# Kernel tuning notes

Hardware: AMD Instinct MI355X
Metric: run time of the kernel (lower is better)

Reference implementation:

```python
import jax, jax.numpy as jnp
import numpy as np

SEQ, BATCH, INPUT = 2048, 64, 16
HEADS, HID = 8, 64  # per-head hidden = hidden_size/output_size = 512/8


def setup_inputs() -> dict:
    key = jax.random.key(0)
    ks = jax.random.split(key, 8)
    s = 1.0 / np.sqrt(HID)  # PyTorch LSTM/Linear init scale
    return {
        "x": jax.random.normal(ks[0], (SEQ, BATCH, INPUT), jnp.float32),
        "W_ih": jax.random.uniform(ks[1], (HEADS, 4 * HID, INPUT), jnp.float32, -s, s),
        "W_hh": jax.random.uniform(ks[2], (HEADS, 4 * HID, HID), jnp.float32, -s, s),
        "b_ih": jax.random.uniform(ks[3], (HEADS, 4 * HID), jnp.float32, -s, s),
        "b_hh": jax.random.uniform(ks[4], (HEADS, 4 * HID), jnp.float32, -s, s),
        "W_lin": jax.random.uniform(ks[5], (HEADS, HID), jnp.float32, -s, s),
        "b_lin": jax.random.uniform(ks[6], (HEADS,), jnp.float32, -s, s),
    }


def _multihead_lstm(x, W_ih, W_hh, b_ih, b_hh):
    # x: (T,B,I); weights stacked over heads H. PyTorch gate order: i,f,g,o.
    T, B = x.shape[0], x.shape[1]
    H, G = W_hh.shape[0], W_hh.shape[1]  # G = 4*hid
    hid = G // 4
    # Input projection for all timesteps/heads at once: (T,B,H,4h)
    xp = jnp.einsum("tbi,hgi->tbhg", x, W_ih) + b_ih + b_hh

    def step(carry, xt):
        h_prev, c_prev = carry  # (B,H,hid)
        z = xt + jnp.einsum("bhk,hgk->bhg", h_prev, W_hh)  # (B,H,4h)
        i = jax.nn.sigmoid(z[..., 0 * hid:1 * hid])
        f = jax.nn.sigmoid(z[..., 1 * hid:2 * hid])
        g = jnp.tanh(z[..., 2 * hid:3 * hid])
        o = jax.nn.sigmoid(z[..., 3 * hid:4 * hid])
        c = f * c_prev + i * g
        h = o * jnp.tanh(c)
        return (h, c), h

    zeros = jnp.zeros((B, H, hid), x.dtype)
    _, hs = jax.lax.scan(step, (zeros, zeros), xp)  # hs: (T,B,H,hid)
    return hs


def reference(x, W_ih, W_hh, b_ih, b_hh, W_lin, b_lin):
    hs = _multihead_lstm(x, W_ih, W_hh, b_ih, b_hh)  # (T,B,H,hid)
    # per-head Linear(hid -> 1), concatenated over heads -> (T,B,H)
    out = jnp.einsum("tbhk,hk->tbh", hs, W_lin) + b_lin
    # lstm_output accumulates (sums) the per-head hidden trajectories
    lstm_output = hs.sum(axis=2)  # (T,B,hid)
    return out, lstm_output
```

## Files before the change

### kernel.cpp

```cpp
#include <hip/hip_runtime.h>
#include <hip/hip_fp16.h>

#define TT   2048
#define BB   64
#define II   16
#define HH   8
#define HIDN 64
#define GG   256
#define T4   (TT / 4)

typedef _Float16 h2 __attribute__((ext_vector_type(2)));
typedef _Float16 h4 __attribute__((ext_vector_type(4)));
typedef _Float16 h8 __attribute__((ext_vector_type(8)));

__device__ __forceinline__ float fdot2(h2 a, h2 b, float c) {
    return __builtin_amdgcn_fdot2(a, b, c, false);
}
__device__ __forceinline__ float fast_sigmoid(float z) {
    return __builtin_amdgcn_rcpf(1.0f + __expf(-z));
}
__device__ __forceinline__ float fast_tanh(float z) {
    return fmaf(2.0f, __builtin_amdgcn_rcpf(1.0f + __expf(-2.0f * z)), -1.0f);
}

__global__ void cvt_x_kernel(const float* __restrict__ x, _Float16* __restrict__ xh, int n4) {
    int i = blockIdx.x * blockDim.x + threadIdx.x;
    if (i < n4) {
        float4 v = ((const float4*)x)[i];
        ((h2*)xh)[2 * i]     = h2{ (_Float16)v.x, (_Float16)v.y };
        ((h2*)xh)[2 * i + 1] = h2{ (_Float16)v.z, (_Float16)v.w };
    }
}

__global__ __launch_bounds__(64, 1)
void lstm_rl(const _Float16* __restrict__ xh,
             const float* __restrict__ Wih,
             const float* __restrict__ Whh,
             const float* __restrict__ bih,
             const float* __restrict__ bhh,
             _Float16* __restrict__ stage_f16)
{
    const int lane = threadIdx.x;
    const int c    = blockIdx.x;
    const int b    = c & (BB - 1);
    const int hd   = c >> 6;
    const bool odd = lane & 1;

    h2 whh[4][HIDN / 2];
    h2 wih[4][II / 2];
    float bias[4];
#pragma unroll
    for (int g = 0; g < 4; ++g) {
        const int r = hd * GG + g * HIDN + lane;
        const float4* p = (const float4*)(Whh + (size_t)r * HIDN);
#pragma unroll
        for (int q = 0; q < HIDN / 4; ++q) {
            float4 v = p[q];
            whh[g][2 * q]     = h2{ (_Float16)v.x, (_Float16)v.y };
            whh[g][2 * q + 1] = h2{ (_Float16)v.z, (_Float16)v.w };
        }
        const float4* pi = (const float4*)(Wih + (size_t)r * II);
#pragma unroll
        for (int q = 0; q < II / 4; ++q) {
            float4 v = pi[q];
            wih[g][2 * q]     = h2{ (_Float16)v.x, (_Float16)v.y };
            wih[g][2 * q + 1] = h2{ (_Float16)v.z, (_Float16)v.w };
        }
        bias[g] = bih[r] + bhh[r];
    }

    float cst   = 0.0f;
    int  packed = 0;

    const _Float16* xhp = xh + b * II;
    h2 xv[II / 2], xn[II / 2];
    auto ldx = [&](int t, h2* dst) {
        const h8* p = (const h8*)(xhp + (size_t)t * BB * II);
        union { h8 v; h2 p2[4]; } u0, u1;
        u0.v = p[0];
        u1.v = p[1];
#pragma unroll
        for (int i = 0; i < 4; ++i) { dst[i] = u0.p2[i]; dst[4 + i] = u1.p2[i]; }
    };
    ldx(0, xv);

    h4* sptr = (h4*)(stage_f16 + (size_t)c * 256 + lane * 4);

    for (int t4 = 0; t4 < T4; ++t4) {
        union { h4 v4; _Float16 e[4]; } hpk;
#pragma unroll
        for (int j = 0; j < 4; ++j) {
            const int t = t4 * 4 + j;
            ldx(t + 1, xn);

            float z0 = bias[0], z1 = bias[1], z2 = bias[2], z3 = bias[3];
#pragma unroll
            for (int q = 0; q < II / 2; ++q) {
                z0 = fdot2(wih[0][q], xv[q], z0);
                z1 = fdot2(wih[1][q], xv[q], z1);
                z2 = fdot2(wih[2][q], xv[q], z2);
                z3 = fdot2(wih[3][q], xv[q], z3);
            }
#pragma unroll
            for (int q = 0; q < HIDN / 2; ++q) {
                h2 hq = __builtin_bit_cast(h2,
                            __builtin_amdgcn_readlane(packed, 2 * q));
                z0 = fdot2(whh[0][q], hq, z0);
                z1 = fdot2(whh[1][q], hq, z1);
                z2 = fdot2(whh[2][q], hq, z2);
                z3 = fdot2(whh[3][q], hq, z3);
            }

            float gi = fast_sigmoid(z0);
            float gf = fast_sigmoid(z1);
            float gg = fast_tanh(z2);
            float go = fast_sigmoid(z3);

            cst = fmaf(gf, cst, gi * gg);
            float hv = go * fast_tanh(cst);
            _Float16 h16 = (_Float16)hv;
            hpk.e[j] = h16;

            int h32 = (int)__builtin_bit_cast(unsigned short, h16);
            int hsw = __builtin_amdgcn_mov_dpp(h32, 0xB1, 0xF, 0xF, true);
            int lo  = odd ? hsw : h32;
            int hi  = odd ? h32 : hsw;
            packed  = lo | (hi << 16);

#pragma unroll
            for (int q = 0; q < II / 2; ++q) xv[q] = xn[q];
        }
        *sptr = hpk.v4;
        sptr += 512 * 64;
    }
}

template <int STAGE, bool XF16>
__global__ __launch_bounds__(64, 1)
void lstm_wave(const float* __restrict__ x,
               const _Float16* __restrict__ xh,
               const float* __restrict__ Wih,
               const float* __restrict__ Whh,
               const float* __restrict__ bih,
               const float* __restrict__ bhh,
               const float* __restrict__ Wlin,
               const float* __restrict__ blin,
               float* __restrict__ out,
               float* __restrict__ lstm_out,
               _Float16* __restrict__ stage_f16)
{
    const int lane = threadIdx.x;
    const int c    = blockIdx.x;
    const int b    = c & (BB - 1);
    const int hd   = c >> 6;

    h2 whh[4][HIDN / 2];
    h2 wih[4][II / 2];
    float bias[4];
#pragma unroll
    for (int g = 0; g < 4; ++g) {
        const int r = hd * GG + g * HIDN + lane;
        const float4* p = (const float4*)(Whh + (size_t)r * HIDN);
#pragma unroll
        for (int q = 0; q < HIDN / 4; ++q) {
            float4 v = p[q];
            whh[g][2 * q]     = h2{ (_Float16)v.x, (_Float16)v.y };
            whh[g][2 * q + 1] = h2{ (_Float16)v.z, (_Float16)v.w };
        }
        const float4* pi = (const float4*)(Wih + (size_t)r * II);
#pragma unroll
        for (int q = 0; q < II / 4; ++q) {
            float4 v = pi[q];
            wih[g][2 * q]     = h2{ (_Float16)v.x, (_Float16)v.y };
            wih[g][2 * q + 1] = h2{ (_Float16)v.z, (_Float16)v.w };
        }
        bias[g] = bih[r] + bhh[r];
    }
    float wl = 0.0f, blv = 0.0f;
    if (STAGE == 2) { wl = Wlin[hd * HIDN + lane]; blv = blin[hd]; }

    __shared__ __align__(16) _Float16 hbuf[HIDN];
    hbuf[lane] = (_Float16)0.0f;

    float cst = 0.0f;

    const _Float16* xhp = xh + b * II;
    const float*    xfp = x + b * II;
    h2 xv[II / 2];
    auto load_x = [&](int t, h2* dst) {
        int tc = t < TT ? t : TT - 1;
        if (XF16) {
            const h8* p = (const h8*)(xhp + (size_t)tc * BB * II);
            union { h8 v; h2 p2[4]; } u0, u1;
            u0.v = p[0];
            u1.v = p[1];
#pragma unroll
            for (int i = 0; i < 4; ++i) { dst[i] = u0.p2[i]; dst[4 + i] = u1.p2[i]; }
        } else {
            const float4* p = (const float4*)(xfp + (size_t)tc * BB * II);
#pragma unroll
            for (int q = 0; q < 4; ++q) {
                float4 v = p[q];
                dst[2 * q]     = h2{ (_Float16)v.x, (_Float16)v.y };
                dst[2 * q + 1] = h2{ (_Float16)v.z, (_Float16)v.w };
            }
        }
    };
    load_x(0, xv);

    h4* sptr = (h4*)(stage_f16 + (size_t)c * 256 + lane * 4);

    for (int t4 = 0; t4 < T4; ++t4) {
        union { h4 v4; h2 p2[2]; } hp;
#pragma unroll
        for (int j = 0; j < 4; ++j) {
            const int t = t4 * 4 + j;
            h2 xn[II / 2];
            load_x(t + 1, xn);

            union { h8 v[8]; h2 p[32]; } hr;
#pragma unroll
            for (int q = 0; q < 8; ++q) hr.v[q] = ((const h8*)hbuf)[q];

            float z0 = bias[0], z1 = bias[1], z2 = bias[2], z3 = bias[3];
#pragma unroll
            for (int q = 0; q < HIDN / 2; ++q) {
                z0 = fdot2(whh[0][q], hr.p[q], z0);
                z1 = fdot2(whh[1][q], hr.p[q], z1);
                z2 = fdot2(whh[2][q], hr.p[q], z2);
                z3 = fdot2(whh[3][q], hr.p[q], z3);
            }
#pragma unroll
            for (int q = 0; q < II / 2; ++q) {
                z0 = fdot2(wih[0][q], xv[q], z0);
                z1 = fdot2(wih[1][q], xv[q], z1);
                z2 = fdot2(wih[2][q], xv[q], z2);
                z3 = fdot2(wih[3][q], xv[q], z3);
            }

            float gi = fast_sigmoid(z0);
            float gf = fast_sigmoid(z1);
            float gg = fast_tanh(z2);
            float go = fast_sigmoid(z3);

            cst = fmaf(gf, cst, gi * gg);
            float h = go * fast_tanh(cst);
            _Float16 h16 = (_Float16)h;

            hbuf[lane] = h16;
            hp.p2[j >> 1][j & 1] = h16;

            if (STAGE == 2) {
                atomicAdd(&lstm_out[((size_t)t * BB + b) * HIDN + lane], h);
                float p = h * wl;
                p += __shfl_down(p, 32, 64);
                p += __shfl_down(p, 16, 64);
                p += __shfl_down(p, 8, 64);
                p += __shfl_down(p, 4, 64);
                p += __shfl_down(p, 2, 64);
                p += __shfl_down(p, 1, 64);
                if (lane == 0) out[((size_t)t * BB + b) * HH + hd] = p + blv;
            }

#pragma unroll
            for (int q = 0; q < II / 2; ++q) xv[q] = xn[q];
        }
        if (STAGE == 1) {
            *sptr = hp.v4;
            sptr += 512 * 64;
        }
    }
}

__global__ __launch_bounds__(256)
void pass_lstm(const _Float16* __restrict__ stage, float* __restrict__ lstm_out)
{
    const int tid  = threadIdx.x;
    const int k    = tid & (HIDN - 1);
    const int q    = tid >> 6;
    const int b    = blockIdx.x & (BB - 1);
    const int tile = blockIdx.x >> 6;
    const h4* sp = (const h4*)stage;

#pragma unroll
    for (int g = 0; g < 4; ++g) {
        const int t4 = tile * 16 + q + 4 * g;
        float acc0 = 0.f, acc1 = 0.f, acc2 = 0.f, acc3 = 0.f;
#pragma unroll
        for (int hd = 0; hd < HH; ++hd) {
            h4 v = sp[((size_t)t4 * 512 + hd * 64 + b) * 64 + k];
            acc0 += (float)v.x; acc1 += (float)v.y;
            acc2 += (float)v.z; acc3 += (float)v.w;
        }
        const size_t t = (size_t)t4 * 4;
        lstm_out[((t + 0) * BB + b) * HIDN + k] = acc0;
        lstm_out[((t + 1) * BB + b) * HIDN + k] = acc1;
        lstm_out[((t + 2) * BB + b) * HIDN + k] = acc2;
        lstm_out[((t + 3) * BB + b) * HIDN + k] = acc3;
    }
}

__global__ __launch_bounds__(512)
void pass_out(const _Float16* __restrict__ stage,
              const float* __restrict__ Wlin,
              const float* __restrict__ blin,
              float* __restrict__ out)
{
    __shared__ float wls[GG * 2];
    const int tid = threadIdx.x;
    wls[tid] = Wlin[tid];
    __syncthreads();

    const int b  = tid >> 3;
    const int hd = tid & 7;
    const int c  = hd * 64 + b;
    const int t4 = blockIdx.x;
    const float bl = blin[hd];

    const h4* sp = (const h4*)stage + ((size_t)t4 * 512 + c) * 64;
    float a0 = 0.f, a1 = 0.f, a2 = 0.f, a3 = 0.f;
#pragma unroll 8
    for (int k = 0; k < HIDN; ++k) {
        h4 v = sp[k];
        float w = wls[hd * HIDN + k];
        a0 = fmaf((float)v.x, w, a0);
        a1 = fmaf((float)v.y, w, a1);
        a2 = fmaf((float)v.z, w, a2);
        a3 = fmaf((float)v.w, w, a3);
    }
    const size_t t = (size_t)t4 * 4;
    out[(t + 0) * 512 + tid] = a0 + bl;
    out[(t + 1) * 512 + tid] = a1 + bl;
    out[(t + 2) * 512 + tid] = a2 + bl;
    out[(t + 3) * 512 + tid] = a3 + bl;
}

extern "C" void kernel_launch(void* const* d_in, const int* in_sizes, int n_in,
                              void* d_out, int out_size, void* d_ws, size_t ws_size,
                              hipStream_t stream)
{
    const float* x    = (const float*)d_in[0];
    const float* Wih  = (const float*)d_in[1];
    const float* Whh  = (const float*)d_in[2];
    const float* bih  = (const float*)d_in[3];
    const float* bhh  = (const float*)d_in[4];
    const float* Wlin = (const float*)d_in[5];
    const float* blin = (const float*)d_in[6];

    float* out  = (float*)d_out;
    float* lstm = out + (size_t)TT * BB * HH;

    const size_t xbytes = (size_t)TT * BB * II * 2 + 4096;
    const size_t slab16 = (size_t)TT * BB * HH * HIDN * 2;

    const bool xf16 = ws_size >= xbytes;
    _Float16* xh = (_Float16*)d_ws;
    char* slabp  = (char*)d_ws + (xf16 ? xbytes : 0);
    size_t avail = ws_size - (xf16 ? xbytes : 0);
    const int mode = (avail >= slab16) ? 1 : 2;

    if (xf16) {
        int n4 = TT * BB * II / 4;
        cvt_x_kernel<<<(n4 + 255) / 256, 256, 0, stream>>>(x, xh, n4);
    }

    _Float16* sh = (_Float16*)slabp;

    if (mode == 1 && xf16) {
        lstm_rl<<<dim3(BB * HH), dim3(64), 0, stream>>>(xh, Wih, Whh, bih, bhh, sh);
        pass_lstm<<<dim3(BB * 32), dim3(256), 0, stream>>>(sh, lstm);
        pass_out <<<dim3(T4), dim3(512), 0, stream>>>(sh, Wlin, blin, out);
    } else if (mode == 1) {
        dim3 grid(BB * HH), block(64);
        lstm_wave<1, false><<<grid, block, 0, stream>>>(x, xh, Wih, Whh, bih, bhh,
                                                        Wlin, blin, out, lstm, sh);
        pass_lstm<<<dim3(BB * 32), dim3(256), 0, stream>>>(sh, lstm);
        pass_out <<<dim3(T4), dim3(512), 0, stream>>>(sh, Wlin, blin, out);
    } else {
        hipMemsetAsync(lstm, 0, (size_t)TT * BB * HIDN * 4, stream);
        dim3 grid(BB * HH), block(64);
        if (xf16)
            lstm_wave<2, true><<<grid, block, 0, stream>>>(x, xh, Wih, Whh, bih, bhh,
                                                           Wlin, blin, out, lstm, sh);
        else
            lstm_wave<2, false><<<grid, block, 0, stream>>>(x, xh, Wih, Whh, bih, bhh,
                                                            Wlin, blin, out, lstm, sh);
    }
}
```

Before: 1.169 ms.

## Broadcast hidden state through LDS and precompute next-step input projection

Replaces the per-step readlane broadcast of the packed hidden state with a write to a small shared-memory buffer that every lane reads back as vector loads. It also computes the next timestep's input projection right after the state update, taking it off the critical recurrence path. The dot-product chains are split into two accumulators to shorten dependency latency. The block pads its LDS to about 64 KB, apparently to limit how many blocks share a CU. The code has no barrier between the LDS write and the next read; it relies on the 64-thread block being a single wavefront executing in lockstep.

Measured after the change: 1.086 ms. 7.1% less time.

```diff
diff --git a/kernel.cpp b/kernel.cpp
--- a/kernel.cpp
+++ b/kernel.cpp
@@ -32,19 +32,25 @@
     }
 }
 
+struct SmemPad {
+    _Float16 hbuf[HIDN];
+    char     pad[63872];
+};
+
 __global__ __launch_bounds__(64, 1)
-void lstm_rl(const _Float16* __restrict__ xh,
-             const float* __restrict__ Wih,
-             const float* __restrict__ Whh,
-             const float* __restrict__ bih,
-             const float* __restrict__ bhh,
-             _Float16* __restrict__ stage_f16)
+void lstm_reg(const _Float16* __restrict__ xh,
+              const float* __restrict__ Wih,
+              const float* __restrict__ Whh,
+              const float* __restrict__ bih,
+              const float* __restrict__ bhh,
+              _Float16* __restrict__ stage_f16)
 {
     const int lane = threadIdx.x;
     const int c    = blockIdx.x;
     const int b    = c & (BB - 1);
     const int hd   = c >> 6;
-    const bool odd = lane & 1;
+
+    __shared__ __align__(16) SmemPad smem;
 
     h2 whh[4][HIDN / 2];
     h2 wih[4][II / 2];
@@ -69,11 +75,13 @@
         bias[g] = bih[r] + bhh[r];
     }
 
-    float cst   = 0.0f;
-    int  packed = 0;
+    smem.hbuf[lane] = (_Float16)0.0f;
+    if (lane == 0) smem.pad[0] = 1;
+
+    float cst = 0.0f;
 
     const _Float16* xhp = xh + b * II;
-    h2 xv[II / 2], xn[II / 2];
+    h2 xn[II / 2];
     auto ldx = [&](int t, h2* dst) {
         const h8* p = (const h8*)(xhp + (size_t)t * BB * II);
         union { h8 v; h2 p2[4]; } u0, u1;
@@ -82,7 +90,19 @@
 #pragma unroll
         for (int i = 0; i < 4; ++i) { dst[i] = u0.p2[i]; dst[4 + i] = u1.p2[i]; }
     };
-    ldx(0, xv);
+
+    float xzA[4], xzB[4];
+    ldx(0, xn);
+#pragma unroll
+    for (int g = 0; g < 4; ++g) { xzA[g] = bias[g]; xzB[g] = 0.0f; }
+#pragma unroll
+    for (int q = 0; q < 4; ++q)
+#pragma unroll
+        for (int g = 0; g < 4; ++g) xzA[g] = fdot2(wih[g][q], xn[q], xzA[g]);
+#pragma unroll
+    for (int q = 4; q < 8; ++q)
+#pragma unroll
+        for (int g = 0; g < 4; ++g) xzB[g] = fdot2(wih[g][q], xn[q], xzB[g]);
 
     h4* sptr = (h4*)(stage_f16 + (size_t)c * 256 + lane * 4);
 
@@ -91,25 +111,31 @@
 #pragma unroll
         for (int j = 0; j < 4; ++j) {
             const int t = t4 * 4 + j;
+
+            union { h8 v[8]; h2 p[32]; } hr;
+#pragma unroll
+            for (int q = 0; q < 8; ++q) hr.v[q] = ((const h8*)smem.hbuf)[q];
+
             ldx(t + 1, xn);
 
-            float z0 = bias[0], z1 = bias[1], z2 = bias[2], z3 = bias[3];
-#pragma unroll
-            for (int q = 0; q < II / 2; ++q) {
-                z0 = fdot2(wih[0][q], xv[q], z0);
-                z1 = fdot2(wih[1][q], xv[q], z1);
-                z2 = fdot2(wih[2][q], xv[q], z2);
-                z3 = fdot2(wih[3][q], xv[q], z3);
-            }
-#pragma unroll
-            for (int q = 0; q < HIDN / 2; ++q) {
-                h2 hq = __builtin_bit_cast(h2,
-                            __builtin_amdgcn_readlane(packed, 2 * q));
-                z0 = fdot2(whh[0][q], hq, z0);
-                z1 = fdot2(whh[1][q], hq, z1);
-                z2 = fdot2(whh[2][q], hq, z2);
-                z3 = fdot2(whh[3][q], hq, z3);
-            }
+            float zA0 = xzA[0], zA1 = xzA[1], zA2 = xzA[2], zA3 = xzA[3];
+            float zB0 = xzB[0], zB1 = xzB[1], zB2 = xzB[2], zB3 = xzB[3];
+#pragma unroll
+            for (int q = 0; q < 16; ++q) {
+                zA0 = fdot2(whh[0][q], hr.p[q], zA0);
+                zA1 = fdot2(whh[1][q], hr.p[q], zA1);
+                zA2 = fdot2(whh[2][q], hr.p[q], zA2);
+                zA3 = fdot2(whh[3][q], hr.p[q], zA3);
+            }
+#pragma unroll
+            for (int q = 16; q < 32; ++q) {
+                zB0 = fdot2(whh[0][q], hr.p[q], zB0);
+                zB1 = fdot2(whh[1][q], hr.p[q], zB1);
+                zB2 = fdot2(whh[2][q], hr.p[q], zB2);
+                zB3 = fdot2(whh[3][q], hr.p[q], zB3);
+            }
+            float z0 = zA0 + zB0, z1 = zA1 + zB1;
+            float z2 = zA2 + zB2, z3 = zA3 + zB3;
 
             float gi = fast_sigmoid(z0);
             float gf = fast_sigmoid(z1);
@@ -119,16 +145,22 @@
             cst = fmaf(gf, cst, gi * gg);
             float hv = go * fast_tanh(cst);
             _Float16 h16 = (_Float16)hv;
+
+            smem.hbuf[lane] = h16;
             hpk.e[j] = h16;
 
-            int h32 = (int)__builtin_bit_cast(unsigned short, h16);
-            int hsw = __builtin_amdgcn_mov_dpp(h32, 0xB1, 0xF, 0xF, true);
-            int lo  = odd ? hsw : h32;
-            int hi  = odd ? h32 : hsw;
-            packed  = lo | (hi << 16);
-
-#pragma unroll
-            for (int q = 0; q < II / 2; ++q) xv[q] = xn[q];
+#pragma unroll
+            for (int g = 0; g < 4; ++g) { xzA[g] = bias[g]; xzB[g] = 0.0f; }
+#pragma unroll
+            for (int q = 0; q < 4; ++q)
+#pragma unroll
+                for (int g = 0; g < 4; ++g)
+                    xzA[g] = fdot2(wih[g][q], xn[q], xzA[g]);
+#pragma unroll
+            for (int q = 4; q < 8; ++q)
+#pragma unroll
+                for (int g = 0; g < 4; ++g)
+                    xzB[g] = fdot2(wih[g][q], xn[q], xzB[g]);
         }
         *sptr = hpk.v4;
         sptr += 512 * 64;
@@ -367,7 +399,7 @@
     _Float16* sh = (_Float16*)slabp;
 
     if (mode == 1 && xf16) {
-        lstm_rl<<<dim3(BB * HH), dim3(64), 0, stream>>>(xh, Wih, Whh, bih, bhh, sh);
+        lstm_reg<<<dim3(BB * HH), dim3(64), 0, stream>>>(xh, Wih, Whh, bih, bhh, sh);
         pass_lstm<<<dim3(BB * 32), dim3(256), 0, stream>>>(sh, lstm);
         pass_out <<<dim3(T4), dim3(512), 0, stream>>>(sh, Wlin, blin, out);
     } else if (mode == 1) {
```
